# Performance work log

Measured on AMD Instinct MI355X. Metric: run time of the kernel, lower is better.

Reference implementation:

```python
import jax, jax.numpy as jnp
import numpy as np

STRIDE = 1

def setup_inputs() -> dict:
    key = jax.random.key(0)
    k1, k2, k3 = jax.random.split(key, 3)
    bs, pep_len, d = 2048, 15, 64
    out_channels, kernel_size, mhc_len = 128, 9, 34
    peptide_x = jax.random.normal(k1, (bs, pep_len, d), dtype=jnp.float32)
    mhc_x = jax.random.normal(k2, (bs, mhc_len, d), dtype=jnp.float32)
    weight = jax.random.normal(k3, (out_channels, kernel_size, mhc_len), dtype=jnp.float32) * 0.02
    bias = jnp.zeros((out_channels,), dtype=jnp.float32)
    return {"peptide_x": peptide_x, "mhc_x": mhc_x, "weight": weight, "bias": bias}

def reference(peptide_x, mhc_x, weight, bias):
    # kernel[n,o,d,k] = relu(sum_l mhc_x[n,l,d] * weight[o,k,l])
    kernel = jax.nn.relu(jnp.einsum('nld,okl->nodk', mhc_x, weight))
    bs, pep_len, d = peptide_x.shape
    ksize = kernel.shape[-1]
    L_out = (pep_len - ksize) // STRIDE + 1
    # sliding windows: [bs, L_out, k, d]
    idx = jnp.arange(L_out)[:, None] * STRIDE + jnp.arange(ksize)[None, :]
    windows = peptide_x[:, idx, :]
    # grouped conv1d (groups=bs) == per-sample contraction over (d, k)
    out = jnp.einsum('ntkd,nodk->not', windows, kernel)
    return out + bias[:, None]
```

## Files before the change

### kernel.cpp

```cpp
#include <hip/hip_runtime.h>

typedef __attribute__((ext_vector_type(8))) short bf16x8;
typedef __attribute__((ext_vector_type(4))) float f32x4;
typedef unsigned short ushort_t;
typedef unsigned int uint_t;

constexpr int PEP = 15;
constexpr int D   = 64;
constexpr int L   = 34;
constexpr int OC  = 128;
constexpr int KS  = 9;
constexpr int TO  = 7;
constexpr int OK  = OC * KS;
constexpr int MTG = OK / 16;
constexpr int NCH = 8;
constexpr int NCHB = 4;
constexpr int CHO = OC / NCH;
constexpr int MT_CH = (CHO * KS) / 16;
constexpr int CTS = 145;
constexpr int SOS = CHO * TO;
constexpr int WP_FRAG = 36864;
constexpr int WP_TAILF = 36864;
constexpr int SMEM_BYTES = 64 * CTS * 4 + 4 * SOS * 4;

__device__ __forceinline__ ushort_t f2bf(float v) {
    uint_t u = __float_as_uint(v);
    return (ushort_t)((u + 0x7fffu + ((u >> 16) & 1u)) >> 16);
}
__device__ __forceinline__ float bf2f(ushort_t h) {
    return __uint_as_float(((uint_t)h) << 16);
}

template <int CTRL>
__device__ __forceinline__ float dpp_shr_add(float v) {
    int x = __builtin_amdgcn_update_dpp(0, __float_as_int(v), CTRL, 0xF, 0xF, true);
    return v + __int_as_float(x);
}

__global__ void wprep_kernel(const float* __restrict__ W, ushort_t* __restrict__ wp) {
    int x = blockIdx.x * 256 + threadIdx.x;
    if (x < 2 * WP_FRAG) {
        int sp = x / WP_FRAG;
        int r  = x % WP_FRAG;
        int i  = r & 7;
        int ln = (r >> 3) & 63;
        int mt = r >> 9;
        int ok = mt * 16 + (ln & 15);
        int l  = (ln >> 4) * 8 + i;
        float v = W[ok * L + l];
        ushort_t hi = f2bf(v);
        wp[x] = sp ? f2bf(v - bf2f(hi)) : hi;
    } else if (x < 2 * WP_FRAG + WP_TAILF) {
        int y  = x - 2 * WP_FRAG;
        int c  = y & 1;
        int j  = (y >> 1) & 3;
        int ln = (y >> 3) & 63;
        int mt = y >> 9;
        int row = mt * 16 + (ln >> 4) * 4 + j;
        ((float*)(wp + 2 * WP_FRAG))[y] = W[row * L + 32 + c];
    }
}

__global__ __launch_bounds__(256, 4) void iconv_mfma(
    const float* __restrict__ pep,
    const float* __restrict__ mhc,
    const ushort_t* __restrict__ wp,
    const float* __restrict__ bias,
    float* __restrict__ out)
{
    __shared__ __align__(16) char smem[SMEM_BYTES];
    const int n    = blockIdx.x;
    const int c0   = blockIdx.y * NCHB;
    const int tid  = threadIdx.x;
    const int lane = tid & 63;
    const int w    = tid >> 6;

    float p[PEP];
    {
        const float* pp = pep + (size_t)n * PEP * D + lane;
        #pragma unroll
        for (int j = 0; j < PEP; ++j) p[j] = pp[j * D];
    }

    float m32v[4], m33v[4];
    {
        const float* mb = mhc + (size_t)n * L * D;
        #pragma unroll
        for (int nt = 0; nt < 4; ++nt) {
            int d = (lane & 15) + 16 * nt;
            m32v[nt] = mb[32 * D + d];
            m33v[nt] = mb[33 * D + d];
        }
    }

    {
        const float* mp = mhc + (size_t)n * L * D + lane;
        #pragma unroll
        for (int j = 0; j < 8; ++j) {
            int l = w + 4 * j;
            float v = mp[l * D];
            ushort_t hi = f2bf(v);
            ushort_t lo = f2bf(v - bf2f(hi));
            int byte = (lane * 128 + l * 2) ^ ((lane & 7) << 4);
            *(ushort_t*)(smem + byte)        = hi;
            *(ushort_t*)(smem + 8192 + byte) = lo;
        }
    }
    __syncthreads();

    bf16x8 bf[4][2];
    #pragma unroll
    for (int nt = 0; nt < 4; ++nt) {
        int d = (lane & 15) + 16 * nt;
        int l0 = (lane >> 4) * 8;
        int byte = (d * 128 + l0 * 2) ^ ((d & 7) << 4);
        bf[nt][0] = *(const bf16x8*)(smem + byte);
        bf[nt][1] = *(const bf16x8*)(smem + 8192 + byte);
    }
    __syncthreads();

    float* CT  = (float*)smem;
    float* so  = (float*)(smem + 64 * CTS * 4);
    float* CTl = CT + lane * CTS;
    const float* wtail = (const float*)(wp + 2 * WP_FRAG);

    auto do_tile = [&](int cg, int mtl) {
        int mtG = cg * MT_CH + mtl;
        const ushort_t* base = wp + mtG * 512 + lane * 8;
        bf16x8 ah = *(const bf16x8*)(base);
        bf16x8 al = *(const bf16x8*)(base + WP_FRAG);
        const float4* tb = (const float4*)(wtail + (size_t)(mtG * 64 + lane) * 8);
        float4 ft0 = tb[0];
        float4 ft1 = tb[1];

        f32x4 acc[4];
        #pragma unroll
        for (int nt = 0; nt < 4; ++nt) acc[nt] = (f32x4){0.f, 0.f, 0.f, 0.f};
        #pragma unroll
        for (int nt = 0; nt < 4; ++nt) {
            acc[nt] = __builtin_amdgcn_mfma_f32_16x16x32_bf16(ah, bf[nt][0], acc[nt], 0, 0, 0);
            acc[nt] = __builtin_amdgcn_mfma_f32_16x16x32_bf16(ah, bf[nt][1], acc[nt], 0, 0, 0);
            acc[nt] = __builtin_amdgcn_mfma_f32_16x16x32_bf16(al, bf[nt][0], acc[nt], 0, 0, 0);
        }
        #pragma unroll
        for (int nt = 0; nt < 4; ++nt) {
            acc[nt][0] = fmaf(ft0.x, m32v[nt], fmaf(ft0.y, m33v[nt], acc[nt][0]));
            acc[nt][1] = fmaf(ft0.z, m32v[nt], fmaf(ft0.w, m33v[nt], acc[nt][1]));
            acc[nt][2] = fmaf(ft1.x, m32v[nt], fmaf(ft1.y, m33v[nt], acc[nt][2]));
            acc[nt][3] = fmaf(ft1.z, m32v[nt], fmaf(ft1.w, m33v[nt], acc[nt][3]));
        }

        int r0 = mtl * 16 + (lane >> 4) * 4;
        #pragma unroll
        for (int nt = 0; nt < 4; ++nt) {
            int d = (lane & 15) + 16 * nt;
            float* dst = CT + d * CTS + r0;
            dst[0] = fmaxf(acc[nt][0], 0.f);
            dst[1] = fmaxf(acc[nt][1], 0.f);
            dst[2] = fmaxf(acc[nt][2], 0.f);
            dst[3] = fmaxf(acc[nt][3], 0.f);
        }
    };

    for (int c = 0; c < NCHB; ++c) {
        const int cg = c0 + c;

        do_tile(cg, w);
        do_tile(cg, w + 4);
        if (w == (cg & 3)) do_tile(cg, 8);
        __syncthreads();

        #pragma unroll
        for (int h = 0; h < 2; ++h) {
            float a2[2][TO];
            #pragma unroll
            for (int oi = 0; oi < 2; ++oi)
                #pragma unroll
                for (int t = 0; t < TO; ++t) a2[oi][t] = 0.f;

            #pragma unroll
            for (int oi = 0; oi < 2; ++oi) {
                const float* row = CTl + (w * 4 + h * 2 + oi) * KS;
                #pragma unroll
                for (int k = 0; k < KS; ++k) {
                    float kk = row[k];
                    #pragma unroll
                    for (int t = 0; t < TO; ++t) a2[oi][t] = fmaf(kk, p[t + k], a2[oi][t]);
                }
            }

            #pragma unroll
            for (int oi = 0; oi < 2; ++oi) {
                #pragma unroll
                for (int t = 0; t < TO; ++t) {
                    float a = a2[oi][t];
                    a = dpp_shr_add<0x111>(a);
                    a = dpp_shr_add<0x112>(a);
                    a = dpp_shr_add<0x114>(a);
                    a = dpp_shr_add<0x118>(a);
                    if ((lane & 15) == 15)
                        so[(lane >> 4) * SOS + (w * 4 + h * 2 + oi) * TO + t] = a;
                }
            }
        }
        __syncthreads();

        if (tid < SOS) {
            int o = cg * CHO + tid / TO;
            float v = (so[tid] + so[SOS + tid]) +
                      (so[2 * SOS + tid] + so[3 * SOS + tid]);
            out[(size_t)n * OC * TO + cg * SOS + tid] = v + bias[o];
        }
    }
}

__global__ __launch_bounds__(256, 4) void iconv_f32(
    const float* __restrict__ pep, const float* __restrict__ mhc,
    const float* __restrict__ wsrc, const float* __restrict__ bias,
    float* __restrict__ out)
{
    __shared__ float so[4 * 900];
    const int n = blockIdx.x, tid = threadIdx.x, lane = tid & 63;
    const int w = __builtin_amdgcn_readfirstlane(tid >> 6);
    float m[L];
    { const float* mp = mhc + (size_t)n * L * D + lane;
      #pragma unroll
      for (int l = 0; l < L; ++l) m[l] = mp[l * D]; }
    float p[PEP];
    { const float* pp = pep + (size_t)n * PEP * D + lane;
      #pragma unroll
      for (int j = 0; j < PEP; ++j) p[j] = pp[j * D]; }
    for (int oo = 0; oo < OC / 4; ++oo) {
        const int o = w * (OC / 4) + oo;
        float acc[TO];
        #pragma unroll
        for (int t = 0; t < TO; ++t) acc[t] = 0.f;
        #pragma unroll
        for (int k = 0; k < KS; ++k) {
            const float2* wrow = reinterpret_cast<const float2*>(wsrc + (size_t)o * KS * L);
            float wr[L];
            #pragma unroll
            for (int q = 0; q < L / 2; ++q) {
                float2 v = wrow[k * (L / 2) + q];
                wr[q * 2] = v.x; wr[q * 2 + 1] = v.y;
            }
            float k0 = 0.f, k1 = 0.f, k2 = 0.f, k3 = 0.f;
            #pragma unroll
            for (int l = 0; l < 32; l += 4) {
                k0 = fmaf(m[l], wr[l], k0);   k1 = fmaf(m[l + 1], wr[l + 1], k1);
                k2 = fmaf(m[l + 2], wr[l + 2], k2); k3 = fmaf(m[l + 3], wr[l + 3], k3);
            }
            k0 = fmaf(m[32], wr[32], k0); k1 = fmaf(m[33], wr[33], k1);
            float kk = fmaxf((k0 + k2) + (k1 + k3), 0.f);
            #pragma unroll
            for (int t = 0; t < TO; ++t) acc[t] = fmaf(p[t + k], kk, acc[t]);
        }
        #pragma unroll
        for (int t = 0; t < TO; ++t) {
            float a = acc[t];
            a += __shfl_xor(a, 1, 64); a += __shfl_xor(a, 2, 64);
            a += __shfl_xor(a, 4, 64); a += __shfl_xor(a, 8, 64);
            if ((lane & 15) == 0) so[(lane >> 4) * 900 + o * TO + t] = a;
        }
    }
    __syncthreads();
    float* on = out + (size_t)n * OC * TO;
    for (int i = tid; i < OC * TO; i += 256) {
        int o = i / TO;
        on[i] = (so[i] + so[900 + i]) + (so[1800 + i] + so[2700 + i]) + bias[o];
    }
}

extern "C" void kernel_launch(void* const* d_in, const int* in_sizes, int n_in,
                              void* d_out, int out_size, void* d_ws, size_t ws_size,
                              hipStream_t stream) {
    const float* pep  = (const float*)d_in[0];
    const float* mhc  = (const float*)d_in[1];
    const float* W    = (const float*)d_in[2];
    const float* bias = (const float*)d_in[3];
    float* out        = (float*)d_out;
    const int bs = in_sizes[0] / (PEP * D);

    const size_t need = 2 * WP_FRAG * sizeof(ushort_t) + WP_TAILF * sizeof(float);
    if (d_ws != nullptr && ws_size >= need) {
        ushort_t* wpx = (ushort_t*)d_ws;
        const int tot = 2 * WP_FRAG + WP_TAILF;
        wprep_kernel<<<(tot + 255) / 256, 256, 0, stream>>>(W, wpx);
        iconv_mfma<<<dim3(bs, 2), 256, 0, stream>>>(pep, mhc, wpx, bias, out);
    } else {
        iconv_f32<<<bs, 256, 0, stream>>>(pep, mhc, W, bias, out);
    }
}
```

Before: 150.3 us.

## Compute per-sample convolution with bf16 MFMA and atomic accumulation into bias-initialised output

The second stage (peptide-window by generated-kernel contraction) moves from scalar FMAs with DPP lane reductions to bf16 MFMA. The generated kernel is stored in LDS as bf16 and the peptide as a hi/lo bf16 split. The k range is split across the four waves, and each wave atomically adds its partial sums into the output. A separate kernel pre-fills the output with the bias. This removes the scalar FMA work, the cross-lane reductions and the final LDS reduction, at the cost of an extra launch, global atomics and lower precision for the kernel values, since relu(einsum) is now rounded to a single bf16 with no lo part.

```diff
diff --git a/kernel.cpp b/kernel.cpp
--- a/kernel.cpp
+++ b/kernel.cpp
@@ -13,15 +13,16 @@
 constexpr int TO  = 7;
 constexpr int OK  = OC * KS;
 constexpr int MTG = OK / 16;
-constexpr int NCH = 8;
 constexpr int NCHB = 4;
-constexpr int CHO = OC / NCH;
-constexpr int MT_CH = (CHO * KS) / 16;
-constexpr int CTS = 145;
-constexpr int SOS = CHO * TO;
+constexpr int CHO = 16;
+constexpr int MT_CH = 9;
+constexpr int CTR = 144;
+constexpr int PPR = 144;
+constexpr int PEPH_OFF = 144 * CTR;
+constexpr int PEPL_OFF = PEPH_OFF + 24 * PPR;
+constexpr int SMEM_BYTES = PEPL_OFF + 24 * PPR;
 constexpr int WP_FRAG = 36864;
 constexpr int WP_TAILF = 36864;
-constexpr int SMEM_BYTES = 64 * CTS * 4 + 4 * SOS * 4;
 
 __device__ __forceinline__ ushort_t f2bf(float v) {
     uint_t u = __float_as_uint(v);
@@ -30,11 +31,10 @@
 __device__ __forceinline__ float bf2f(ushort_t h) {
     return __uint_as_float(((uint_t)h) << 16);
 }
-
-template <int CTRL>
-__device__ __forceinline__ float dpp_shr_add(float v) {
-    int x = __builtin_amdgcn_update_dpp(0, __float_as_int(v), CTRL, 0xF, 0xF, true);
-    return v + __int_as_float(x);
+__device__ __forceinline__ uint_t cvt_pk_bf16(float a, float b) {
+    uint_t r;
+    asm("v_cvt_pk_bf16_f32 %0, %1, %2" : "=v"(r) : "v"(a), "v"(b));
+    return r;
 }
 
 __global__ void wprep_kernel(const float* __restrict__ W, ushort_t* __restrict__ wp) {
@@ -61,11 +61,15 @@
     }
 }
 
+__global__ void oinit_kernel(const float* __restrict__ bias, float* __restrict__ out, int total) {
+    int i = blockIdx.x * 256 + threadIdx.x;
+    if (i < total) out[i] = bias[(i % (OC * TO)) / TO];
+}
+
 __global__ __launch_bounds__(256, 4) void iconv_mfma(
     const float* __restrict__ pep,
     const float* __restrict__ mhc,
     const ushort_t* __restrict__ wp,
-    const float* __restrict__ bias,
     float* __restrict__ out)
 {
     __shared__ __align__(16) char smem[SMEM_BYTES];
@@ -75,13 +79,6 @@
     const int lane = tid & 63;
     const int w    = tid >> 6;
 
-    float p[PEP];
-    {
-        const float* pp = pep + (size_t)n * PEP * D + lane;
-        #pragma unroll
-        for (int j = 0; j < PEP; ++j) p[j] = pp[j * D];
-    }
-
     float m32v[4], m33v[4];
     {
         const float* mb = mhc + (size_t)n * L * D;
@@ -106,6 +103,19 @@
             *(ushort_t*)(smem + 8192 + byte) = lo;
         }
     }
+    {
+        const float* pp = pep + (size_t)n * PEP * D + lane;
+        #pragma unroll
+        for (int j = 0; j < 6; ++j) {
+            int r = w + 4 * j;
+            float v = (r < PEP) ? pp[r * D] : 0.0f;
+            ushort_t hi = f2bf(v);
+            ushort_t lo = f2bf(v - bf2f(hi));
+            int byte = r * PPR + lane * 2;
+            *(ushort_t*)(smem + PEPH_OFF + byte) = hi;
+            *(ushort_t*)(smem + PEPL_OFF + byte) = lo;
+        }
+    }
     __syncthreads();
 
     bf16x8 bf[4][2];
@@ -119,9 +129,6 @@
     }
     __syncthreads();
 
-    float* CT  = (float*)smem;
-    float* so  = (float*)(smem + 64 * CTS * 4);
-    float* CTl = CT + lane * CTS;
     const float* wtail = (const float*)(wp + 2 * WP_FRAG);
 
     auto do_tile = [&](int cg, int mtl) {
@@ -153,12 +160,13 @@
         int r0 = mtl * 16 + (lane >> 4) * 4;
         #pragma unroll
         for (int nt = 0; nt < 4; ++nt) {
-            int d = (lane & 15) + 16 * nt;
-            float* dst = CT + d * CTS + r0;
-            dst[0] = fmaxf(acc[nt][0], 0.f);
-            dst[1] = fmaxf(acc[nt][1], 0.f);
-            dst[2] = fmaxf(acc[nt][2], 0.f);
-            dst[3] = fmaxf(acc[nt][3], 0.f);
+            int bb = ((lane & 15) + 16 * nt) * 2;
+            uint_t w01 = cvt_pk_bf16(fmaxf(acc[nt][0], 0.f), fmaxf(acc[nt][1], 0.f));
+            uint_t w23 = cvt_pk_bf16(fmaxf(acc[nt][2], 0.f), fmaxf(acc[nt][3], 0.f));
+            *(ushort_t*)(smem + (r0 + 0) * CTR + bb) = (ushort_t)(w01 & 0xffffu);
+            *(ushort_t*)(smem + (r0 + 1) * CTR + bb) = (ushort_t)(w01 >> 16);
+            *(ushort_t*)(smem + (r0 + 2) * CTR + bb) = (ushort_t)(w23 & 0xffffu);
+            *(ushort_t*)(smem + (r0 + 3) * CTR + bb) = (ushort_t)(w23 >> 16);
         }
     };
 
@@ -170,47 +178,36 @@
         if (w == (cg & 3)) do_tile(cg, 8);
         __syncthreads();
 
-        #pragma unroll
-        for (int h = 0; h < 2; ++h) {
-            float a2[2][TO];
-            #pragma unroll
-            for (int oi = 0; oi < 2; ++oi)
-                #pragma unroll
-                for (int t = 0; t < TO; ++t) a2[oi][t] = 0.f;
-
-            #pragma unroll
-            for (int oi = 0; oi < 2; ++oi) {
-                const float* row = CTl + (w * 4 + h * 2 + oi) * KS;
-                #pragma unroll
-                for (int k = 0; k < KS; ++k) {
-                    float kk = row[k];
-                    #pragma unroll
-                    for (int t = 0; t < TO; ++t) a2[oi][t] = fmaf(kk, p[t + k], a2[oi][t]);
-                }
-            }
-
-            #pragma unroll
-            for (int oi = 0; oi < 2; ++oi) {
-                #pragma unroll
-                for (int t = 0; t < TO; ++t) {
-                    float a = a2[oi][t];
-                    a = dpp_shr_add<0x111>(a);
-                    a = dpp_shr_add<0x112>(a);
-                    a = dpp_shr_add<0x114>(a);
-                    a = dpp_shr_add<0x118>(a);
-                    if ((lane & 15) == 15)
-                        so[(lane >> 4) * SOS + (w * 4 + h * 2 + oi) * TO + t] = a;
-                }
+        const int rot  = (cg + 1) & 3;
+        const int idx  = (w - rot) & 3;
+        const int kbeg = (idx == 0) ? 0 : (idx == 1) ? 3 : (idx == 2) ? 5 : 7;
+        const int kcnt = (idx == 0) ? 3 : 2;
+        const int gg   = (lane >> 4) * 16;
+
+        f32x4 acc2 = (f32x4){0.f, 0.f, 0.f, 0.f};
+        for (int kk = 0; kk < kcnt; ++kk) {
+            int k = kbeg + kk;
+            int pbase = ((lane & 15) + k) * PPR + gg;
+            int cbase = ((lane & 15) * KS + k) * CTR + gg;
+            #pragma unroll
+            for (int dh = 0; dh < 2; ++dh) {
+                bf16x8 phi = *(const bf16x8*)(smem + PEPH_OFF + pbase + dh * 64);
+                bf16x8 plo = *(const bf16x8*)(smem + PEPL_OFF + pbase + dh * 64);
+                bf16x8 khi = *(const bf16x8*)(smem + cbase + dh * 64);
+                acc2 = __builtin_amdgcn_mfma_f32_16x16x32_bf16(phi, khi, acc2, 0, 0, 0);
+                acc2 = __builtin_amdgcn_mfma_f32_16x16x32_bf16(plo, khi, acc2, 0, 0, 0);
+            }
+        }
+        {
+            int t0 = (lane >> 4) * 4;
+            float* ob = out + (size_t)n * (OC * TO) + cg * (CHO * TO) + (lane & 15) * TO;
+            #pragma unroll
+            for (int r2 = 0; r2 < 4; ++r2) {
+                int t = t0 + r2;
+                if (t < TO) unsafeAtomicAdd(ob + t, acc2[r2]);
             }
         }
         __syncthreads();
-
-        if (tid < SOS) {
-            int o = cg * CHO + tid / TO;
-            float v = (so[tid] + so[SOS + tid]) +
-                      (so[2 * SOS + tid] + so[3 * SOS + tid]);
-            out[(size_t)n * OC * TO + cg * SOS + tid] = v + bias[o];
-        }
     }
 }
 
@@ -286,7 +283,9 @@
         ushort_t* wpx = (ushort_t*)d_ws;
         const int tot = 2 * WP_FRAG + WP_TAILF;
         wprep_kernel<<<(tot + 255) / 256, 256, 0, stream>>>(W, wpx);
-        iconv_mfma<<<dim3(bs, 2), 256, 0, stream>>>(pep, mhc, wpx, bias, out);
+        const int ototal = bs * OC * TO;
+        oinit_kernel<<<(ototal + 255) / 256, 256, 0, stream>>>(bias, out, ototal);
+        iconv_mfma<<<dim3(bs, 2), 256, 0, stream>>>(pep, mhc, wpx, out);
     } else {
         iconv_f32<<<bs, 256, 0, stream>>>(pep, mhc, W, bias, out);
     }
```

Result: slower. 200.5 us (+33.5%).
